# Kernel optimization log

Measured on AMD Instinct MI355X. Metric: run time of the kernel, lower is better.

Reference implementation:

```python
import jax, jax.numpy as jnp
import numpy as np

CUTOFF = 2.0
LOG2 = float(np.log(2.0))

def ssp(x):
    # shifted softplus: softplus(x) - log(2)
    return jax.nn.softplus(x) - LOG2

def setup_inputs() -> dict:
    key = jax.random.key(0)
    ks = jax.random.split(key, 12)
    N, E, H, F, G = 10000, 320000, 256, 256, 50
    x = jax.random.normal(ks[0], (N, H), dtype=jnp.float32)
    edge_index = jax.random.randint(ks[1], (2, E), 0, N, dtype=jnp.int64)
    edge_weight = jax.random.normal(ks[2], (E, 3), dtype=jnp.float32)
    edge_attr = jax.random.normal(ks[3], (E, G), dtype=jnp.float32)
    s = lambda fan_in: 1.0 / np.sqrt(fan_in)
    mlp_w1 = jax.random.uniform(ks[4], (G, F), jnp.float32, -s(G), s(G))
    mlp_b1 = jax.random.uniform(ks[5], (F,), jnp.float32, -s(G), s(G))
    mlp_w2 = jax.random.uniform(ks[6], (F, F), jnp.float32, -s(F), s(F))
    mlp_b2 = jax.random.uniform(ks[7], (F,), jnp.float32, -s(F), s(F))
    lin1_w = jax.random.uniform(ks[8], (H, F), jnp.float32, -s(H), s(H))
    lin2_w = jax.random.uniform(ks[9], (F, H), jnp.float32, -s(F), s(F))
    lin2_b = jax.random.uniform(ks[10], (H,), jnp.float32, -s(F), s(F))
    return {"x": x, "edge_index": edge_index, "edge_weight": edge_weight,
            "edge_attr": edge_attr, "mlp_w1": mlp_w1, "mlp_b1": mlp_b1,
            "mlp_w2": mlp_w2, "mlp_b2": mlp_b2, "lin1_w": lin1_w,
            "lin2_w": lin2_w, "lin2_b": lin2_b}

def reference(x, edge_index, edge_weight, edge_attr,
              mlp_w1, mlp_b1, mlp_w2, mlp_b2, lin1_w, lin2_w, lin2_b):
    N = x.shape[0]
    # cutoff envelope on edge distances
    distances = jnp.linalg.norm(edge_weight, axis=1)                 # [E]
    C = 0.5 * (jnp.cos(distances * jnp.pi / CUTOFF) + 1.0)
    C = C * (distances <= CUTOFF)                                    # [E]
    # edge filter MLP
    W = ssp(edge_attr @ mlp_w1 + mlp_b1) @ mlp_w2 + mlp_b2           # [E, F]
    W = W * C[:, None]
    i, j = edge_index[0], edge_index[1]
    messages = W * (x[j] @ lin1_w)                                   # [E, F]
    agg = jax.ops.segment_sum(messages, i, num_segments=N)           # [N, F]
    h = ssp(agg @ lin2_w + lin2_b)                                   # [N, H]
    return x + h
```

## Files before the change

kernel.cpp:

```cpp
#include <hip/hip_runtime.h>
#include <hip/hip_bf16.h>
#include <stdint.h>

#define HF 256
#define GG 50

typedef __attribute__((ext_vector_type(8))) short bf16x8;
typedef __attribute__((ext_vector_type(4))) short bf16x4;
typedef __attribute__((ext_vector_type(4))) float f32x4;

__device__ __forceinline__ uint32_t f2bf2u(float a, float b){
    __hip_bfloat162 h = __float22bfloat162_rn(make_float2(a, b));
    union { __hip_bfloat162 h; uint32_t u; } v; v.h = h; return v.u;
}
__device__ __forceinline__ float bf2f(short s){
    union { uint32_t u; float f; } v; v.u = ((uint32_t)(uint16_t)s) << 16;
    return v.f;
}
__device__ __forceinline__ float ssp_f(float x){
    float e = __builtin_amdgcn_exp2f(x * 1.44269504088896341f);
    return 0.69314718055994531f * __builtin_amdgcn_logf(1.0f + e)
         - 0.69314718055994531f;
}

__device__ __forceinline__ void pack_natural(const float* __restrict__ B,
                                             short* __restrict__ Bp,
                                             int idx, int KT, int kmax)
{
    int lane = idx & 63;
    int kt   = (idx >> 6) & (KT - 1);
    int ntg  = idx >> (6 + (KT == 2 ? 1 : 3));
    int col  = ntg * 16 + (lane & 15);
    int k0   = kt * 32 + (lane >> 4) * 8;
    uint32_t u[4];
#pragma unroll
    for (int jj = 0; jj < 4; ++jj) {
        int ka = k0 + 2*jj, kb = ka + 1;
        float a = (ka < kmax) ? B[(size_t)ka * HF + col] : 0.f;
        float b = (kb < kmax) ? B[(size_t)kb * HF + col] : 0.f;
        u[jj] = f2bf2u(a, b);
    }
    *(uint4*)&Bp[(size_t)idx * 8] = *(uint4*)u;
}

__global__ __launch_bounds__(256)
void prep_kernel(const float* __restrict__ w1, const float* __restrict__ b1,
                 const float* __restrict__ w2,
                 const float* __restrict__ lin1, const float* __restrict__ lin2,
                 short* __restrict__ w1p, short* __restrict__ w2p,
                 short* __restrict__ lin1p, short* __restrict__ lin2p,
                 const float* __restrict__ x, short* __restrict__ x_bf, int nx8,
                 const int* __restrict__ eidx, int* __restrict__ cnt, int E,
                 float* __restrict__ agg, int nAgg4, int gConv, int gHist)
{
    int b = blockIdx.x, tid = threadIdx.x;
    if (b < 8) {
        int idx  = b * 256 + tid;
        int lane = idx & 63;
        int kt   = (idx >> 6) & 1;
        int ntg  = idx >> 7;
        int col  = ntg * 16 + (lane & 15);
        int k0   = kt * 32 + (lane >> 4) * 8;
        uint32_t u[4];
#pragma unroll
        for (int jj = 0; jj < 4; ++jj) {
            int ka = k0 + 2*jj, kb = ka + 1;
            float va = (ka < GG) ? w1[(size_t)ka * HF + col]
                                 : ((ka == GG) ? b1[col] : 0.f);
            float vb = (kb < GG) ? w1[(size_t)kb * HF + col]
                                 : ((kb == GG) ? b1[col] : 0.f);
            u[jj] = f2bf2u(va, vb);
        }
        *(uint4*)&w1p[(size_t)idx * 8] = *(uint4*)u;
    } else if (b < 40) {
        int idx = (b - 8) * 256 + tid;
        int lane = idx & 63;
        int kt   = (idx >> 6) & 7;
        int ntg  = idx >> 9;
        int col  = ntg * 16 + (lane & 15);
        int s0   = kt * 32 + (lane >> 4) * 8;
        uint32_t u[4];
#pragma unroll
        for (int jj = 0; jj < 4; ++jj) {
            int sa = s0 + 2*jj, sb = sa + 1;
            int fa = (sa >> 5) * 32 + (sa & 1) * 16 + ((sa & 31) >> 1);
            int fb = (sb >> 5) * 32 + (sb & 1) * 16 + ((sb & 31) >> 1);
            u[jj] = f2bf2u(w2[(size_t)fa * HF + col], w2[(size_t)fb * HF + col]);
        }
        *(uint4*)&w2p[(size_t)idx * 8] = *(uint4*)u;
    } else if (b < 72) {
        pack_natural(lin1, lin1p, (b - 40) * 256 + tid, 8, HF);
    } else if (b < 104) {
        pack_natural(lin2, lin2p, (b - 72) * 256 + tid, 8, HF);
    } else if (b < 104 + gConv) {
        int idx = (b - 104) * 256 + tid;
        if (idx < nx8) {
            const float* xp = x + (size_t)idx * 8;
            float4 p0 = *(const float4*)(xp);
            float4 p1 = *(const float4*)(xp + 4);
            uint32_t u[4] = { f2bf2u(p0.x, p0.y), f2bf2u(p0.z, p0.w),
                              f2bf2u(p1.x, p1.y), f2bf2u(p1.z, p1.w) };
            *(uint4*)&x_bf[(size_t)idx * 8] = *(uint4*)u;
        }
    } else if (b < 104 + gConv + gHist) {
        int e = (b - 104 - gConv) * 256 + tid;
        if (e < E) atomicAdd(&cnt[eidx[e]], 1);
    } else {
        int idx = (b - 104 - gConv - gHist) * 256 + tid;
        if (idx < nAgg4) ((float4*)agg)[idx] = make_float4(0.f, 0.f, 0.f, 0.f);
    }
}

__global__ __launch_bounds__(256)
void scan_kernel(const int* __restrict__ cnt, int* __restrict__ row,
                 int* __restrict__ cursor, int N, int E)
{
    __shared__ int part[256];
    const int t = threadIdx.x;
    const int CH = (N + 255) / 256;
    int lo = t * CH;
    int hi = min(lo + CH, N);
    int s = 0;
    for (int n = lo; n < hi; ++n) s += cnt[n];
    part[t] = s;
    __syncthreads();
    for (int off = 1; off < 256; off <<= 1) {
        int v = (t >= off) ? part[t - off] : 0;
        __syncthreads();
        part[t] += v;
        __syncthreads();
    }
    int acc = part[t] - s;
    for (int n = lo; n < hi; ++n) {
        row[n] = acc; cursor[n] = acc;
        acc += cnt[n];
    }
    if (t == 255) row[N] = E;
}

__global__ __launch_bounds__(256)
void mid_kernel(const int* __restrict__ eidx, int* __restrict__ cursor,
                int* __restrict__ perm, int E, int gScatter,
                const short* __restrict__ x_bf, const short* __restrict__ lin1p,
                short* __restrict__ y_p, int N)
{
    const int tid = threadIdx.x;
    if ((int)blockIdx.x < gScatter) {
        int e = blockIdx.x * 256 + tid;
        if (e < E) {
            int pos = atomicAdd(&cursor[eidx[e]], 1);
            perm[pos] = e;
        }
        return;
    }
    const int blk  = blockIdx.x - gScatter;
    const int lane = tid & 63;
    const int w    = tid >> 6;
    const int l15  = lane & 15;
    const int quad = lane >> 4;
    const int row0 = blk * 64;

    f32x4 acc[4][4];
#pragma unroll
    for (int mt = 0; mt < 4; ++mt)
#pragma unroll
        for (int nt = 0; nt < 4; ++nt) acc[mt][nt] = (f32x4){0.f,0.f,0.f,0.f};

#pragma unroll 2
    for (int kt = 0; kt < 8; ++kt) {
        bf16x8 af[4];
#pragma unroll
        for (int mt = 0; mt < 4; ++mt) {
            int r = row0 + mt * 16 + l15;
            int rl = (r < N) ? r : 0;
            af[mt] = *(const bf16x8*)&x_bf[(size_t)rl * HF + kt * 32 + quad * 8];
        }
#pragma unroll
        for (int nt = 0; nt < 4; ++nt) {
            bf16x8 bfr = *(const bf16x8*)&lin1p[(size_t)(((w*4+nt)*8+kt)*64+lane)*8];
#pragma unroll
            for (int mt = 0; mt < 4; ++mt)
                acc[mt][nt] = __builtin_amdgcn_mfma_f32_16x16x32_bf16(af[mt], bfr, acc[mt][nt], 0, 0, 0);
        }
    }
#pragma unroll
    for (int mt = 0; mt < 4; ++mt) {
#pragma unroll
        for (int r = 0; r < 4; ++r) {
            int row = row0 + mt * 16 + quad * 4 + r;
            if (row < N) {
                uint2 u = make_uint2(f2bf2u(acc[mt][0][r], acc[mt][1][r]),
                                     f2bf2u(acc[mt][2][r], acc[mt][3][r]));
                *(uint2*)&y_p[(size_t)row * HF + w * 64 + l15 * 4] = u;
            }
        }
    }
}

__global__ __launch_bounds__(256)
void node2_kernel(const float* __restrict__ agg, const short* __restrict__ lin2p,
                  const float* __restrict__ bias, const float* __restrict__ x,
                  float* __restrict__ out, int N)
{
    const int tid  = threadIdx.x;
    const int lane = tid & 63;
    const int w    = tid >> 6;
    const int l15  = lane & 15;
    const int quad = lane >> 4;
    const int row0 = blockIdx.x * 64;

    f32x4 acc[4][4];
#pragma unroll
    for (int mt = 0; mt < 4; ++mt)
#pragma unroll
        for (int nt = 0; nt < 4; ++nt) acc[mt][nt] = (f32x4){0.f,0.f,0.f,0.f};

#pragma unroll 2
    for (int kt = 0; kt < 8; ++kt) {
        bf16x8 af[4];
#pragma unroll
        for (int mt = 0; mt < 4; ++mt) {
            int r = row0 + mt * 16 + l15;
            int rl = (r < N) ? r : 0;
            const float* ap = agg + (size_t)rl * HF + kt * 32 + quad * 8;
            float4 p0 = *(const float4*)(ap);
            float4 p1 = *(const float4*)(ap + 4);
            union { uint32_t u[4]; bf16x8 v; } c;
            c.u[0] = f2bf2u(p0.x, p0.y); c.u[1] = f2bf2u(p0.z, p0.w);
            c.u[2] = f2bf2u(p1.x, p1.y); c.u[3] = f2bf2u(p1.z, p1.w);
            af[mt] = c.v;
        }
#pragma unroll
        for (int nt = 0; nt < 4; ++nt) {
            bf16x8 bfr = *(const bf16x8*)&lin2p[(size_t)(((w*4+nt)*8+kt)*64+lane)*8];
#pragma unroll
            for (int mt = 0; mt < 4; ++mt)
                acc[mt][nt] = __builtin_amdgcn_mfma_f32_16x16x32_bf16(af[mt], bfr, acc[mt][nt], 0, 0, 0);
        }
    }
    float bs[4];
#pragma unroll
    for (int nt = 0; nt < 4; ++nt) bs[nt] = bias[w * 64 + nt * 16 + l15];
#pragma unroll
    for (int mt = 0; mt < 4; ++mt) {
#pragma unroll
        for (int r = 0; r < 4; ++r) {
            int row = row0 + mt * 16 + quad * 4 + r;
            if (row < N) {
#pragma unroll
                for (int nt = 0; nt < 4; ++nt) {
                    int f = w * 64 + nt * 16 + l15;
                    float v = ssp_f(acc[mt][nt][r] + bs[nt]) + x[(size_t)row * HF + f];
                    out[(size_t)row * HF + f] = v;
                }
            }
        }
    }
}

__global__ __launch_bounds__(512, 6)
void edge_mfma(const float* __restrict__ ea, const int* __restrict__ eidx,
               const float* __restrict__ ew,
               const short* __restrict__ w1p,
               const short* __restrict__ w2p, const float* __restrict__ b2,
               const short* __restrict__ y_p, const int* __restrict__ perm,
               const int* __restrict__ rowp,
               float* __restrict__ agg, int E)
{
    __shared__ short smem[19584];
    short* ea_b = smem;
    short* hid  = smem;
    short* msgT = smem;
    short* St   = smem + 18432;
    __shared__ int s_e[64], s_j[64];
    __shared__ float s_c[64];
    __shared__ int s_runnode[64];
    __shared__ unsigned char s_runcomp[64];
    __shared__ unsigned long long s_bmask;
    __shared__ int s_runcnt;

    const int tid  = threadIdx.x;
    const int lane = tid & 63;
    const int w    = tid >> 6;
    const int l15  = lane & 15;
    const int quad = lane >> 4;
    const int e0   = blockIdx.x * 64;

    if (tid < 64) {
        int pp = e0 + tid;
        int e = 0, iv = -1, jv = 0;
        float c = 0.f;
        if (pp < E) {
            e  = perm[pp];
            iv = eidx[e];
            jv = eidx[E + e];
            float d0 = ew[e*3+0], d1 = ew[e*3+1], d2 = ew[e*3+2];
            float d = sqrtf(d0*d0 + d1*d1 + d2*d2);
            c = (d <= 2.0f) ? 0.5f * (__cosf(d * 1.57079632679489662f) + 1.0f) : 0.f;
        }
        s_e[tid] = e; s_j[tid] = jv; s_c[tid] = c;
        int ivn = __shfl_down(iv, 1);
        bool flag = (tid == 63) || (iv != ivn);
        unsigned long long m = __ballot(flag);
        if (flag) {
            int rid = (int)__popcll(m & ((1ull << tid) - 1ull));
            s_runnode[rid] = iv;
            int comp = 0;
            if (iv >= 0) {
                int lo = rowp[iv], hi = rowp[iv + 1];
                comp = (lo >= e0 && hi <= e0 + 64) ? 1 : 0;
            }
            s_runcomp[rid] = (unsigned char)comp;
        }
        if (tid == 0) { s_bmask = m; s_runcnt = (int)__popcll(m); }
    }
    __syncthreads();

    for (int idx = tid; idx < 64 * 25; idx += 512) {
        int e = idx / 25, q = idx - e * 25;
        const float* sp = ea + (size_t)s_e[e] * GG + q * 2;
        float2 v = *(const float2*)sp;
        *(uint32_t*)&ea_b[e * 72 + q * 2] = f2bf2u(v.x, v.y);
    }
    for (int idx = tid; idx < 64 * 7; idx += 512) {
        int e = idx / 7, q = idx - e * 7;
        *(uint32_t*)&ea_b[e * 72 + 50 + q * 2] = (q == 0) ? 0x00003F80u : 0u;
    }
    __syncthreads();

    f32x4 acc1[4][2];
#pragma unroll
    for (int mt = 0; mt < 4; ++mt)
#pragma unroll
        for (int nt = 0; nt < 2; ++nt) acc1[mt][nt] = (f32x4){0.f,0.f,0.f,0.f};

#pragma unroll
    for (int kt = 0; kt < 2; ++kt) {
        bf16x8 af[4];
#pragma unroll
        for (int mt = 0; mt < 4; ++mt)
            af[mt] = *(bf16x8*)&ea_b[(mt * 16 + l15) * 72 + kt * 32 + quad * 8];
#pragma unroll
        for (int nt = 0; nt < 2; ++nt) {
            bf16x8 bfr = *(const bf16x8*)&w1p[(size_t)(((w*2+nt)*2+kt)*64+lane)*8];
#pragma unroll
            for (int mt = 0; mt < 4; ++mt)
                acc1[mt][nt] = __builtin_amdgcn_mfma_f32_16x16x32_bf16(af[mt], bfr, acc1[mt][nt], 0, 0, 0);
        }
    }
    __syncthreads();

#pragma unroll
    for (int mt = 0; mt < 4; ++mt) {
#pragma unroll
        for (int r = 0; r < 4; ++r) {
            int e = mt * 16 + quad * 4 + r;
            float v0 = ssp_f(acc1[mt][0][r]);
            float v1 = ssp_f(acc1[mt][1][r]);
            *(uint32_t*)&hid[e * 264 + w * 32 + l15 * 2] = f2bf2u(v0, v1);
        }
    }
    __syncthreads();

    f32x4 acc2[4][2];
#pragma unroll
    for (int mt = 0; mt < 4; ++mt)
#pragma unroll
        for (int nt = 0; nt < 2; ++nt) acc2[mt][nt] = (f32x4){0.f,0.f,0.f,0.f};

    __builtin_amdgcn_s_setprio(1);
#pragma unroll 1
    for (int kt = 0; kt < 8; ++kt) {
        bf16x8 af[4];
#pragma unroll
        for (int mt = 0; mt < 4; ++mt)
            af[mt] = *(bf16x8*)&hid[(mt * 16 + l15) * 264 + kt * 32 + quad * 8];
#pragma unroll
        for (int nt = 0; nt < 2; ++nt) {
            bf16x8 bfr = *(const bf16x8*)&w2p[(size_t)(((w*2+nt)*8+kt)*64+lane)*8];
#pragma unroll
            for (int mt = 0; mt < 4; ++mt)
                acc2[mt][nt] = __builtin_amdgcn_mfma_f32_16x16x32_bf16(af[mt], bfr, acc2[mt][nt], 0, 0, 0);
        }
    }
    __builtin_amdgcn_s_setprio(0);

    uint32_t yv[4][4];
    const int ypos = (w >> 1) * 64 + l15 * 4 + (w & 1) * 2;
#pragma unroll
    for (int mt = 0; mt < 4; ++mt)
#pragma unroll
        for (int r = 0; r < 4; ++r) {
            int e = mt * 16 + quad * 4 + r;
            yv[mt][r] = *(const uint32_t*)&y_p[(size_t)s_j[e] * HF + ypos];
        }
    float bias2[2];
#pragma unroll
    for (int nt = 0; nt < 2; ++nt) bias2[nt] = b2[w * 32 + nt * 16 + l15];

    __syncthreads();

#pragma unroll
    for (int mt = 0; mt < 4; ++mt) {
        float c0 = s_c[mt * 16 + quad * 4 + 0];
        float c1 = s_c[mt * 16 + quad * 4 + 1];
        float c2 = s_c[mt * 16 + quad * 4 + 2];
        float c3 = s_c[mt * 16 + quad * 4 + 3];
#pragma unroll
        for (int nt = 0; nt < 2; ++nt) {
            int col = w * 32 + nt * 16 + l15;
            float y0 = bf2f((short)(nt ? (yv[mt][0] >> 16) : (yv[mt][0] & 0xFFFF)));
            float y1 = bf2f((short)(nt ? (yv[mt][1] >> 16) : (yv[mt][1] & 0xFFFF)));
            float y2 = bf2f((short)(nt ? (yv[mt][2] >> 16) : (yv[mt][2] & 0xFFFF)));
            float y3 = bf2f((short)(nt ? (yv[mt][3] >> 16) : (yv[mt][3] & 0xFFFF)));
            float v0 = (acc2[mt][nt][0] + bias2[nt]) * c0 * y0;
            float v1 = (acc2[mt][nt][1] + bias2[nt]) * c1 * y1;
            float v2 = (acc2[mt][nt][2] + bias2[nt]) * c2 * y2;
            float v3 = (acc2[mt][nt][3] + bias2[nt]) * c3 * y3;
            uint2 u = make_uint2(f2bf2u(v0, v1), f2bf2u(v2, v3));
            *(uint2*)&msgT[col * 72 + mt * 16 + quad * 4] = u;
        }
    }
    {
        unsigned long long bm = s_bmask;
        int e   = tid & 63;
        int rb  = tid >> 6;
        int rid = (int)__popcll(bm & ((1ull << e) - 1ull));
#pragma unroll
        for (int q = 0; q < 2; ++q) {
            int r = rb + q * 8;
            St[r * 72 + e] = (rid == r) ? (short)0x3F80 : (short)0;
        }
    }
    __syncthreads();

    const int runcnt = s_runcnt;
    for (int ntg = 0; ntg * 16 < runcnt; ++ntg) {
        if (ntg > 0) {
            __syncthreads();
            unsigned long long bm = s_bmask;
            int e   = tid & 63;
            int rb  = tid >> 6;
            int rid = (int)__popcll(bm & ((1ull << e) - 1ull));
#pragma unroll
            for (int q = 0; q < 2; ++q) {
                int r = rb + q * 8;
                St[r * 72 + e] = (rid == ntg * 16 + r) ? (short)0x3F80 : (short)0;
            }
            __syncthreads();
        }
        f32x4 acc3[2];
#pragma unroll
        for (int mt = 0; mt < 2; ++mt) acc3[mt] = (f32x4){0.f,0.f,0.f,0.f};
#pragma unroll
        for (int kt = 0; kt < 2; ++kt) {
            bf16x8 bS = *(bf16x8*)&St[l15 * 72 + kt * 32 + quad * 8];
#pragma unroll
            for (int mt = 0; mt < 2; ++mt) {
                bf16x8 af = *(bf16x8*)&msgT[(w*32 + mt*16 + l15) * 72 + kt*32 + quad*8];
                acc3[mt] = __builtin_amdgcn_mfma_f32_16x16x32_bf16(af, bS, acc3[mt], 0, 0, 0);
            }
        }
        int r = ntg * 16 + l15;
        if (r < runcnt) {
            int node = s_runnode[r];
            if (node >= 0) {
                float* ap = agg + (size_t)node * HF + w * 32 + quad * 4;
                if (s_runcomp[r]) {
#pragma unroll
                    for (int mt = 0; mt < 2; ++mt) {
                        float4 v = make_float4(acc3[mt][0], acc3[mt][1], acc3[mt][2], acc3[mt][3]);
                        *(float4*)(ap + mt * 16) = v;
                    }
                } else {
#pragma unroll
                    for (int mt = 0; mt < 2; ++mt)
#pragma unroll
                        for (int g = 0; g < 4; ++g)
                            atomicAdd(ap + mt * 16 + g, acc3[mt][g]);
                }
            }
        }
    }
}

extern "C" void kernel_launch(void* const* d_in, const int* in_sizes, int n_in,
                              void* d_out, int out_size, void* d_ws, size_t ws_size,
                              hipStream_t stream)
{
    const float* x     = (const float*)d_in[0];
    const int*   eidx  = (const int*)  d_in[1];
    const float* ew    = (const float*)d_in[2];
    const float* ea    = (const float*)d_in[3];
    const float* w1    = (const float*)d_in[4];
    const float* b1    = (const float*)d_in[5];
    const float* w2    = (const float*)d_in[6];
    const float* b2    = (const float*)d_in[7];
    const float* lin1  = (const float*)d_in[8];
    const float* lin2  = (const float*)d_in[9];
    const float* lin2b = (const float*)d_in[10];
    float* out = (float*)d_out;

    const int N = in_sizes[0] / HF;
    const int E = in_sizes[2] / 3;

    const size_t fN = (size_t)N * HF;
    float* agg    = (float*)d_ws;
    short* y_p    = (short*)(agg + fN);
    short* x_bf   = y_p + fN;
    int*   cnt    = (int*)(x_bf + fN);
    int*   row    = cnt + N;
    int*   cursor = row + (N + 8);
    int*   perm   = cursor + N;
    short* w1p    = (short*)(((uintptr_t)(perm + E) + 255) & ~(uintptr_t)255);
    short* w2p    = w1p + 16384;
    short* lin1p  = w2p + 65536;
    short* lin2p  = lin1p + 65536;

    hipMemsetAsync(cnt, 0, (size_t)N * sizeof(int), stream);

    const int nx8   = (int)(fN / 8);
    const int nAgg4 = (int)(fN / 4);
    const int gConv = (nx8 + 255) / 256;
    const int gHist = (E + 255) / 256;
    const int gZero = (nAgg4 + 255) / 256;
    prep_kernel<<<dim3(104 + gConv + gHist + gZero), dim3(256), 0, stream>>>(
        w1, b1, w2, lin1, lin2, w1p, w2p, lin1p, lin2p, x, x_bf, nx8,
        eidx, cnt, E, agg, nAgg4, gConv, gHist);

    scan_kernel<<<dim3(1), dim3(256), 0, stream>>>(cnt, row, cursor, N, E);

    const int gScatter = (E + 255) / 256;
    const int gNode    = (N + 63) / 64;
    mid_kernel<<<dim3(gScatter + gNode), dim3(256), 0, stream>>>(
        eidx, cursor, perm, E, gScatter, x_bf, lin1p, y_p, N);

    edge_mfma<<<dim3((E + 63) / 64), dim3(512), 0, stream>>>(
        ea, eidx, ew, w1p, w2p, b2, y_p, perm, row, agg, E);

    node2_kernel<<<dim3(gNode), dim3(256), 0, stream>>>(
        agg, lin2p, lin2b, x, out, N);
}
```

Measured before the change: 317.7 us.

## Fold softplus constants into packed weights and rebalance node GEMM kernels

Folds log2(e) into w1, b1 and lin2, and ln2 into w2, so the softplus activations use raw exp2/log with no extra multiplies. The -ln2 shift of the hidden activation is moved into a precomputed corrected bias b2p, built from the bf16-rounded scaled w2. The x@lin1 GEMM now runs alongside the CSR scan in one kernel, and the edge scatter gets its own launch. The node GEMMs are split across two column halves so twice as many blocks run with fewer accumulators each, and the edge_attr staging loop is flattened into one unrolled pass. The cost is an extra kernel launch and small changes to rounding.

```diff
diff --git a/kernel.cpp b/kernel.cpp
--- a/kernel.cpp
+++ b/kernel.cpp
@@ -4,6 +4,8 @@
 
 #define HF 256
 #define GG 50
+#define LOG2E 1.44269504088896341f
+#define LN2   0.69314718055994531f
 
 typedef __attribute__((ext_vector_type(8))) short bf16x8;
 typedef __attribute__((ext_vector_type(4))) short bf16x4;
@@ -17,15 +19,10 @@
     union { uint32_t u; float f; } v; v.u = ((uint32_t)(uint16_t)s) << 16;
     return v.f;
 }
-__device__ __forceinline__ float ssp_f(float x){
-    float e = __builtin_amdgcn_exp2f(x * 1.44269504088896341f);
-    return 0.69314718055994531f * __builtin_amdgcn_logf(1.0f + e)
-         - 0.69314718055994531f;
-}
 
 __device__ __forceinline__ void pack_natural(const float* __restrict__ B,
                                              short* __restrict__ Bp,
-                                             int idx, int KT, int kmax)
+                                             int idx, int KT, int kmax, float scale)
 {
     int lane = idx & 63;
     int kt   = (idx >> 6) & (KT - 1);
@@ -36,8 +33,8 @@
 #pragma unroll
     for (int jj = 0; jj < 4; ++jj) {
         int ka = k0 + 2*jj, kb = ka + 1;
-        float a = (ka < kmax) ? B[(size_t)ka * HF + col] : 0.f;
-        float b = (kb < kmax) ? B[(size_t)kb * HF + col] : 0.f;
+        float a = (ka < kmax) ? B[(size_t)ka * HF + col] * scale : 0.f;
+        float b = (kb < kmax) ? B[(size_t)kb * HF + col] * scale : 0.f;
         u[jj] = f2bf2u(a, b);
     }
     *(uint4*)&Bp[(size_t)idx * 8] = *(uint4*)u;
@@ -45,10 +42,11 @@
 
 __global__ __launch_bounds__(256)
 void prep_kernel(const float* __restrict__ w1, const float* __restrict__ b1,
-                 const float* __restrict__ w2,
+                 const float* __restrict__ w2, const float* __restrict__ b2,
                  const float* __restrict__ lin1, const float* __restrict__ lin2,
                  short* __restrict__ w1p, short* __restrict__ w2p,
                  short* __restrict__ lin1p, short* __restrict__ lin2p,
+                 float* __restrict__ b2p,
                  const float* __restrict__ x, short* __restrict__ x_bf, int nx8,
                  const int* __restrict__ eidx, int* __restrict__ cnt, int E,
                  float* __restrict__ agg, int nAgg4, int gConv, int gHist)
@@ -65,10 +63,10 @@
 #pragma unroll
         for (int jj = 0; jj < 4; ++jj) {
             int ka = k0 + 2*jj, kb = ka + 1;
-            float va = (ka < GG) ? w1[(size_t)ka * HF + col]
-                                 : ((ka == GG) ? b1[col] : 0.f);
-            float vb = (kb < GG) ? w1[(size_t)kb * HF + col]
-                                 : ((kb == GG) ? b1[col] : 0.f);
+            float va = (ka < GG) ? w1[(size_t)ka * HF + col] * LOG2E
+                                 : ((ka == GG) ? b1[col] * LOG2E : 0.f);
+            float vb = (kb < GG) ? w1[(size_t)kb * HF + col] * LOG2E
+                                 : ((kb == GG) ? b1[col] * LOG2E : 0.f);
             u[jj] = f2bf2u(va, vb);
         }
         *(uint4*)&w1p[(size_t)idx * 8] = *(uint4*)u;
@@ -85,15 +83,24 @@
             int sa = s0 + 2*jj, sb = sa + 1;
             int fa = (sa >> 5) * 32 + (sa & 1) * 16 + ((sa & 31) >> 1);
             int fb = (sb >> 5) * 32 + (sb & 1) * 16 + ((sb & 31) >> 1);
-            u[jj] = f2bf2u(w2[(size_t)fa * HF + col], w2[(size_t)fb * HF + col]);
+            u[jj] = f2bf2u(w2[(size_t)fa * HF + col] * LN2,
+                           w2[(size_t)fb * HF + col] * LN2);
         }
         *(uint4*)&w2p[(size_t)idx * 8] = *(uint4*)u;
     } else if (b < 72) {
-        pack_natural(lin1, lin1p, (b - 40) * 256 + tid, 8, HF);
+        pack_natural(lin1, lin1p, (b - 40) * 256 + tid, 8, HF, 1.0f);
     } else if (b < 104) {
-        pack_natural(lin2, lin2p, (b - 72) * 256 + tid, 8, HF);
-    } else if (b < 104 + gConv) {
-        int idx = (b - 104) * 256 + tid;
+        pack_natural(lin2, lin2p, (b - 72) * 256 + tid, 8, HF, LOG2E);
+    } else if (b == 104) {
+        int f = tid;
+        float s = 0.f;
+        for (int k = 0; k < HF; ++k) {
+            uint32_t r = f2bf2u(w2[(size_t)k * HF + f] * LN2, 0.f);
+            s += bf2f((short)(r & 0xFFFF));
+        }
+        b2p[f] = b2[f] - s;
+    } else if (b < 105 + gConv) {
+        int idx = (b - 105) * 256 + tid;
         if (idx < nx8) {
             const float* xp = x + (size_t)idx * 8;
             float4 p0 = *(const float4*)(xp);
@@ -102,69 +109,59 @@
                               f2bf2u(p1.x, p1.y), f2bf2u(p1.z, p1.w) };
             *(uint4*)&x_bf[(size_t)idx * 8] = *(uint4*)u;
         }
-    } else if (b < 104 + gConv + gHist) {
-        int e = (b - 104 - gConv) * 256 + tid;
+    } else if (b < 105 + gConv + gHist) {
+        int e = (b - 105 - gConv) * 256 + tid;
         if (e < E) atomicAdd(&cnt[eidx[e]], 1);
     } else {
-        int idx = (b - 104 - gConv - gHist) * 256 + tid;
+        int idx = (b - 105 - gConv - gHist) * 256 + tid;
         if (idx < nAgg4) ((float4*)agg)[idx] = make_float4(0.f, 0.f, 0.f, 0.f);
     }
 }
 
 __global__ __launch_bounds__(256)
-void scan_kernel(const int* __restrict__ cnt, int* __restrict__ row,
-                 int* __restrict__ cursor, int N, int E)
-{
-    __shared__ int part[256];
-    const int t = threadIdx.x;
-    const int CH = (N + 255) / 256;
-    int lo = t * CH;
-    int hi = min(lo + CH, N);
-    int s = 0;
-    for (int n = lo; n < hi; ++n) s += cnt[n];
-    part[t] = s;
-    __syncthreads();
-    for (int off = 1; off < 256; off <<= 1) {
-        int v = (t >= off) ? part[t - off] : 0;
+void scan_gemm_kernel(const int* __restrict__ cnt, int* __restrict__ row,
+                      int* __restrict__ cursor, int N, int E,
+                      const short* __restrict__ x_bf, const short* __restrict__ lin1p,
+                      short* __restrict__ y_p)
+{
+    const int tid = threadIdx.x;
+    if (blockIdx.x == 0) {
+        __shared__ int part[256];
+        const int CH = (N + 255) / 256;
+        int lo = tid * CH;
+        int hi = min(lo + CH, N);
+        int s = 0;
+        for (int n = lo; n < hi; ++n) s += cnt[n];
+        part[tid] = s;
         __syncthreads();
-        part[t] += v;
-        __syncthreads();
-    }
-    int acc = part[t] - s;
-    for (int n = lo; n < hi; ++n) {
-        row[n] = acc; cursor[n] = acc;
-        acc += cnt[n];
-    }
-    if (t == 255) row[N] = E;
-}
-
-__global__ __launch_bounds__(256)
-void mid_kernel(const int* __restrict__ eidx, int* __restrict__ cursor,
-                int* __restrict__ perm, int E, int gScatter,
-                const short* __restrict__ x_bf, const short* __restrict__ lin1p,
-                short* __restrict__ y_p, int N)
-{
-    const int tid = threadIdx.x;
-    if ((int)blockIdx.x < gScatter) {
-        int e = blockIdx.x * 256 + tid;
-        if (e < E) {
-            int pos = atomicAdd(&cursor[eidx[e]], 1);
-            perm[pos] = e;
-        }
+        for (int off = 1; off < 256; off <<= 1) {
+            int v = (tid >= off) ? part[tid - off] : 0;
+            __syncthreads();
+            part[tid] += v;
+            __syncthreads();
+        }
+        int acc = part[tid] - s;
+        for (int n = lo; n < hi; ++n) {
+            row[n] = acc; cursor[n] = acc;
+            acc += cnt[n];
+        }
+        if (tid == 255) row[N] = E;
         return;
     }
-    const int blk  = blockIdx.x - gScatter;
+    const int blk    = blockIdx.x - 1;
+    const int rowblk = blk >> 1;
+    const int fh     = blk & 1;
     const int lane = tid & 63;
     const int w    = tid >> 6;
     const int l15  = lane & 15;
     const int quad = lane >> 4;
-    const int row0 = blk * 64;
-
-    f32x4 acc[4][4];
+    const int row0 = rowblk * 64;
+
+    f32x4 acc[4][2];
 #pragma unroll
     for (int mt = 0; mt < 4; ++mt)
 #pragma unroll
-        for (int nt = 0; nt < 4; ++nt) acc[mt][nt] = (f32x4){0.f,0.f,0.f,0.f};
+        for (int nt = 0; nt < 2; ++nt) acc[mt][nt] = (f32x4){0.f,0.f,0.f,0.f};
 
 #pragma unroll 2
     for (int kt = 0; kt < 8; ++kt) {
@@ -176,24 +173,36 @@
             af[mt] = *(const bf16x8*)&x_bf[(size_t)rl * HF + kt * 32 + quad * 8];
         }
 #pragma unroll
-        for (int nt = 0; nt < 4; ++nt) {
-            bf16x8 bfr = *(const bf16x8*)&lin1p[(size_t)(((w*4+nt)*8+kt)*64+lane)*8];
+        for (int nt = 0; nt < 2; ++nt) {
+            int ntg = fh * 8 + w * 2 + nt;
+            bf16x8 bfr = *(const bf16x8*)&lin1p[(size_t)((ntg*8+kt)*64+lane)*8];
 #pragma unroll
             for (int mt = 0; mt < 4; ++mt)
                 acc[mt][nt] = __builtin_amdgcn_mfma_f32_16x16x32_bf16(af[mt], bfr, acc[mt][nt], 0, 0, 0);
         }
     }
+    const int sbase = (fh * 2 + (w >> 1)) * 64 + l15 * 4 + (w & 1) * 2;
 #pragma unroll
     for (int mt = 0; mt < 4; ++mt) {
 #pragma unroll
         for (int r = 0; r < 4; ++r) {
-            int row = row0 + mt * 16 + quad * 4 + r;
-            if (row < N) {
-                uint2 u = make_uint2(f2bf2u(acc[mt][0][r], acc[mt][1][r]),
-                                     f2bf2u(acc[mt][2][r], acc[mt][3][r]));
-                *(uint2*)&y_p[(size_t)row * HF + w * 64 + l15 * 4] = u;
+            int row_ = row0 + mt * 16 + quad * 4 + r;
+            if (row_ < N) {
+                *(uint32_t*)&y_p[(size_t)row_ * HF + sbase] =
+                    f2bf2u(acc[mt][0][r], acc[mt][1][r]);
             }
         }
+    }
+}
+
+__global__ __launch_bounds__(256)
+void scatter_kernel(const int* __restrict__ eidx, int* __restrict__ cursor,
+                    int* __restrict__ perm, int E)
+{
+    int e = blockIdx.x * 256 + threadIdx.x;
+    if (e < E) {
+        int pos = atomicAdd(&cursor[eidx[e]], 1);
+        perm[pos] = e;
     }
 }
 
@@ -207,13 +216,14 @@
     const int w    = tid >> 6;
     const int l15  = lane & 15;
     const int quad = lane >> 4;
-    const int row0 = blockIdx.x * 64;
-
-    f32x4 acc[4][4];
+    const int row0 = ((int)blockIdx.x >> 1) * 64;
+    const int fh   = blockIdx.x & 1;
+
+    f32x4 acc[4][2];
 #pragma unroll
     for (int mt = 0; mt < 4; ++mt)
 #pragma unroll
-        for (int nt = 0; nt < 4; ++nt) acc[mt][nt] = (f32x4){0.f,0.f,0.f,0.f};
+        for (int nt = 0; nt < 2; ++nt) acc[mt][nt] = (f32x4){0.f,0.f,0.f,0.f};
 
 #pragma unroll 2
     for (int kt = 0; kt < 8; ++kt) {
@@ -231,16 +241,18 @@
             af[mt] = c.v;
         }
 #pragma unroll
-        for (int nt = 0; nt < 4; ++nt) {
-            bf16x8 bfr = *(const bf16x8*)&lin2p[(size_t)(((w*4+nt)*8+kt)*64+lane)*8];
+        for (int nt = 0; nt < 2; ++nt) {
+            int ntg = fh * 8 + w * 2 + nt;
+            bf16x8 bfr = *(const bf16x8*)&lin2p[(size_t)((ntg*8+kt)*64+lane)*8];
 #pragma unroll
             for (int mt = 0; mt < 4; ++mt)
                 acc[mt][nt] = __builtin_amdgcn_mfma_f32_16x16x32_bf16(af[mt], bfr, acc[mt][nt], 0, 0, 0);
         }
     }
-    float bs[4];
-#pragma unroll
-    for (int nt = 0; nt < 4; ++nt) bs[nt] = bias[w * 64 + nt * 16 + l15];
+    float bs[2];
+#pragma unroll
+    for (int nt = 0; nt < 2; ++nt)
+        bs[nt] = LOG2E * bias[fh * 128 + w * 32 + nt * 16 + l15];
 #pragma unroll
     for (int mt = 0; mt < 4; ++mt) {
 #pragma unroll
@@ -248,10 +260,12 @@
             int row = row0 + mt * 16 + quad * 4 + r;
             if (row < N) {
 #pragma unroll
-                for (int nt = 0; nt < 4; ++nt) {
-                    int f = w * 64 + nt * 16 + l15;
-                    float v = ssp_f(acc[mt][nt][r] + bs[nt]) + x[(size_t)row * HF + f];
-                    out[(size_t)row * HF + f] = v;
+                for (int nt = 0; nt < 2; ++nt) {
+                    int f = fh * 128 + w * 32 + nt * 16 + l15;
+                    float z = acc[mt][nt][r] + bs[nt];
+                    float g = __builtin_amdgcn_logf(1.f + __builtin_amdgcn_exp2f(z));
+                    float xv = x[(size_t)row * HF + f];
+                    out[(size_t)row * HF + f] = fmaf(LN2, g, xv - LN2);
                 }
             }
         }
@@ -262,7 +276,7 @@
 void edge_mfma(const float* __restrict__ ea, const int* __restrict__ eidx,
                const float* __restrict__ ew,
                const short* __restrict__ w1p,
-               const short* __restrict__ w2p, const float* __restrict__ b2,
+               const short* __restrict__ w2p, const float* __restrict__ b2p,
                const short* __restrict__ y_p, const int* __restrict__ perm,
                const int* __restrict__ rowp,
                float* __restrict__ agg, int E)
@@ -316,15 +330,18 @@
     }
     __syncthreads();
 
-    for (int idx = tid; idx < 64 * 25; idx += 512) {
-        int e = idx / 25, q = idx - e * 25;
-        const float* sp = ea + (size_t)s_e[e] * GG + q * 2;
-        float2 v = *(const float2*)sp;
-        *(uint32_t*)&ea_b[e * 72 + q * 2] = f2bf2u(v.x, v.y);
-    }
-    for (int idx = tid; idx < 64 * 7; idx += 512) {
-        int e = idx / 7, q = idx - e * 7;
-        *(uint32_t*)&ea_b[e * 72 + 50 + q * 2] = (q == 0) ? 0x00003F80u : 0u;
+#pragma unroll
+    for (int i = 0; i < 4; ++i) {
+        int idx = i * 512 + tid;
+        int e = idx >> 5, q = idx & 31;
+        uint32_t val;
+        if (q < 25) {
+            float2 v = *(const float2*)(ea + (size_t)s_e[e] * GG + q * 2);
+            val = f2bf2u(v.x, v.y);
+        } else {
+            val = (q == 25) ? 0x00003F80u : 0u;
+        }
+        *(uint32_t*)&ea_b[e * 72 + q * 2] = val;
     }
     __syncthreads();
 
@@ -355,9 +372,9 @@
 #pragma unroll
         for (int r = 0; r < 4; ++r) {
             int e = mt * 16 + quad * 4 + r;
-            float v0 = ssp_f(acc1[mt][0][r]);
-            float v1 = ssp_f(acc1[mt][1][r]);
-            *(uint32_t*)&hid[e * 264 + w * 32 + l15 * 2] = f2bf2u(v0, v1);
+            float g0 = __builtin_amdgcn_logf(1.f + __builtin_amdgcn_exp2f(acc1[mt][0][r]));
+            float g1 = __builtin_amdgcn_logf(1.f + __builtin_amdgcn_exp2f(acc1[mt][1][r]));
+            *(uint32_t*)&hid[e * 264 + w * 32 + l15 * 2] = f2bf2u(g0, g1);
         }
     }
     __syncthreads();
@@ -396,7 +413,7 @@
         }
     float bias2[2];
 #pragma unroll
-    for (int nt = 0; nt < 2; ++nt) bias2[nt] = b2[w * 32 + nt * 16 + l15];
+    for (int nt = 0; nt < 2; ++nt) bias2[nt] = b2p[w * 32 + nt * 16 + l15];
 
     __syncthreads();
 
@@ -516,6 +533,7 @@
     short* w2p    = w1p + 16384;
     short* lin1p  = w2p + 65536;
     short* lin2p  = lin1p + 65536;
+    float* b2p    = (float*)(lin2p + 65536);
 
     hipMemsetAsync(cnt, 0, (size_t)N * sizeof(int), stream);
 
@@ -524,20 +542,20 @@
     const int gConv = (nx8 + 255) / 256;
     const int gHist = (E + 255) / 256;
     const int gZero = (nAgg4 + 255) / 256;
-    prep_kernel<<<dim3(104 + gConv + gHist + gZero), dim3(256), 0, stream>>>(
-        w1, b1, w2, lin1, lin2, w1p, w2p, lin1p, lin2p, x, x_bf, nx8,
-        eidx, cnt, E, agg, nAgg4, gConv, gHist);
-
-    scan_kernel<<<dim3(1), dim3(256), 0, stream>>>(cnt, row, cursor, N, E);
+    prep_kernel<<<dim3(105 + gConv + gHist + gZero), dim3(256), 0, stream>>>(
+        w1, b1, w2, b2, lin1, lin2, w1p, w2p, lin1p, lin2p, b2p,
+        x, x_bf, nx8, eidx, cnt, E, agg, nAgg4, gConv, gHist);
+
+    const int gNode = (N + 63) / 64;
+    scan_gemm_kernel<<<dim3(1 + 2 * gNode), dim3(256), 0, stream>>>(
+        cnt, row, cursor, N, E, x_bf, lin1p, y_p);
 
     const int gScatter = (E + 255) / 256;
-    const int gNode    = (N + 63) / 64;
-    mid_kernel<<<dim3(gScatter + gNode), dim3(256), 0, stream>>>(
-        eidx, cursor, perm, E, gScatter, x_bf, lin1p, y_p, N);
+    scatter_kernel<<<dim3(gScatter), dim3(256), 0, stream>>>(eidx, cursor, perm, E);
 
     edge_mfma<<<dim3((E + 63) / 64), dim3(512), 0, stream>>>(
-        ea, eidx, ew, w1p, w2p, b2, y_p, perm, row, agg, E);
-
-    node2_kernel<<<dim3(gNode), dim3(256), 0, stream>>>(
+        ea, eidx, ew, w1p, w2p, b2p, y_p, perm, row, agg, E);
+
+    node2_kernel<<<dim3(2 * gNode), dim3(256), 0, stream>>>(
         agg, lin2p, lin2b, x, out, N);
 }
```

New measurement: 325.0 us. 2.3% more time.
